# Kernel tuning notes

Hardware: AMD Instinct MI355X
Metric: run time of the kernel (lower is better)

The kernel has to match this reference:

```python
import jax, jax.numpy as jnp
import numpy as np

L, H, DH, D, F, BLK, VOCAB = 2, 16, 128, 2048, 8192, 64, 32000
B, S, R = 16, 77, 16
LORA_SCALE = 32.0 / 16.0  # alpha / r

# standard bitsandbytes NF4 codebook
NF4 = jnp.array([-1.0, -0.6961928009986877, -0.5250730514526367,
                 -0.39491748809814453, -0.28444138169288635, -0.18477343022823334,
                 -0.09105003625154495, 0.0, 0.07958029955625534, 0.16093020141124725,
                 0.24611230194568634, 0.33791524171829224, 0.44070982933044434,
                 0.5626170039176941, 0.723855197429657, 1.0], dtype=jnp.float32)


def setup_inputs() -> dict:
    key = jax.random.key(0)
    ks = jax.random.split(key, 24)
    n = lambda k, sh, s=0.02: jax.random.normal(k, sh, jnp.float32) * s
    u = lambda k, sh: jax.random.uniform(k, sh, dtype=jnp.float32) * 0.02
    ri = lambda k, sh, hi: jax.random.randint(k, sh, 0, hi, jnp.int32)
    return {
        "input_ids": ri(ks[0], (B, S), VOCAB),
        "attention_mask": jnp.ones((B, S), jnp.int32),
        "embed": n(ks[1], (VOCAB, D)),
        "ln_attn": jnp.ones((L, D), jnp.float32),
        "ln_mlp": jnp.ones((L, D), jnp.float32),
        "ln_final": jnp.ones((D,), jnp.float32),
        "qkv_codes": ri(ks[2], (L, 3, D, D), 16),
        "qkv_absmax": u(ks[3], (L, 3, D, D // BLK)),
        "qkv_A": n(ks[4], (L, 3, R, D)),
        "qkv_B": n(ks[5], (L, 3, D, R), 0.01),
        "o_codes": ri(ks[6], (L, D, D), 16),
        "o_absmax": u(ks[7], (L, D, D // BLK)),
        "o_A": n(ks[8], (L, R, D)),
        "o_B": n(ks[9], (L, D, R), 0.01),
        "gu_codes": ri(ks[10], (L, 2, F, D), 16),
        "gu_absmax": u(ks[11], (L, 2, F, D // BLK)),
        "gu_A": n(ks[12], (L, 2, R, D)),
        "gu_B": n(ks[13], (L, 2, F, R), 0.01),
        "down_codes": ri(ks[14], (L, D, F), 16),
        "down_absmax": u(ks[15], (L, D, F // BLK)),
        "down_A": n(ks[16], (L, R, F)),
        "down_B": n(ks[17], (L, D, R), 0.01),
    }


def _rmsnorm(x, w, eps=1e-6):
    return x * jax.lax.rsqrt(jnp.mean(x * x, axis=-1, keepdims=True) + eps) * w


def _dequant(codes, absmax):
    # codes: (out, cin) ints in [0,16); absmax: (out, cin//BLK) blockwise scales
    out, cin = codes.shape
    w = NF4[codes].reshape(out, cin // BLK, BLK) * absmax[..., None]
    return w.reshape(out, cin)


def _qlora(x, codes, absmax, A, Bm):
    # NF4 dequant base matmul + rank-R LoRA delta (eval mode, no dropout)
    W = _dequant(codes, absmax)
    return x @ W.T + LORA_SCALE * ((x @ A.T) @ Bm.T)


def _rope_cache(seq):
    inv = 1.0 / (10000.0 ** (jnp.arange(0, DH, 2, dtype=jnp.float32) / DH))
    f = jnp.arange(seq, dtype=jnp.float32)[:, None] * inv  # (S, DH/2)
    emb = jnp.concatenate([f, f], axis=-1)                 # (S, DH)
    return jnp.cos(emb), jnp.sin(emb)


def _rope(x, cos, sin):
    # x: (B, H, S, DH), llama-style rotate_half
    x1, x2 = jnp.split(x, 2, axis=-1)
    return x * cos + jnp.concatenate([-x2, x1], axis=-1) * sin


def _forward(input_ids, attention_mask, embed, ln_attn, ln_mlp, ln_final,
             qkv_codes, qkv_absmax, qkv_A, qkv_B,
             o_codes, o_absmax, o_A, o_B,
             gu_codes, gu_absmax, gu_A, gu_B,
             down_codes, down_absmax, down_A, down_B):
    b, s = input_ids.shape
    h = embed[input_ids]                                    # (B, S, D)
    cos, sin = _rope_cache(s)
    pad = attention_mask.astype(bool)[:, None, None, :]     # (B,1,1,S)
    mask = pad & jnp.tril(jnp.ones((s, s), bool))
    inv_sqrt_dh = np.float32(1.0 / np.sqrt(DH))
    for l in range(L):
        x = _rmsnorm(h, ln_attn[l])
        q, k, v = [_qlora(x, qkv_codes[l, i], qkv_absmax[l, i], qkv_A[l, i], qkv_B[l, i])
                   .reshape(b, s, H, DH).transpose(0, 2, 1, 3) for i in range(3)]
        q, k = _rope(q, cos, sin), _rope(k, cos, sin)
        scores = jnp.einsum('bhqd,bhkd->bhqk', q, k) * inv_sqrt_dh
        attn = jax.nn.softmax(jnp.where(mask, scores, -1e9), axis=-1)
        o = jnp.einsum('bhqk,bhkd->bhqd', attn, v).transpose(0, 2, 1, 3).reshape(b, s, D)
        h = h + _qlora(o, o_codes[l], o_absmax[l], o_A[l], o_B[l])
        x = _rmsnorm(h, ln_mlp[l])
        g = _qlora(x, gu_codes[l, 0], gu_absmax[l, 0], gu_A[l, 0], gu_B[l, 0])
        up = _qlora(x, gu_codes[l, 1], gu_absmax[l, 1], gu_A[l, 1], gu_B[l, 1])
        h = h + _qlora(jax.nn.silu(g) * up,
                       down_codes[l], down_absmax[l], down_A[l], down_B[l])
    h = _rmsnorm(h, ln_final)
    lengths = attention_mask.sum(axis=1) - 1                # last non-pad token index
    return h[jnp.arange(b), lengths]                        # (B, D)


def reference(input_ids, attention_mask, embed, ln_attn, ln_mlp, ln_final,
              qkv_codes, qkv_absmax, qkv_A, qkv_B,
              o_codes, o_absmax, o_A, o_B,
              gu_codes, gu_absmax, gu_A, gu_B,
              down_codes, down_absmax, down_A, down_B):
    return _forward(input_ids, attention_mask, embed, ln_attn, ln_mlp, ln_final,
                    qkv_codes, qkv_absmax, qkv_A, qkv_B,
                    o_codes, o_absmax, o_A, o_B,
                    gu_codes, gu_absmax, gu_A, gu_B,
                    down_codes, down_absmax, down_A, down_B)
```

## Files before the change

kernel.cpp:

```cpp
#include <hip/hip_runtime.h>
#include <cstdint>
#include <cstddef>

#define M_TOK   1232
#define M_PAD   1280
#define D_MODEL 2048
#define F_FFN   8192
#define SEQ     77
#define BATCH   16
#define NHEAD   16
#define LRANK   16
#define NLAYER  2
#define ATILE   16
#define MWB     512

typedef short bf16x8 __attribute__((ext_vector_type(8)));
typedef float f32x4  __attribute__((ext_vector_type(4)));

__device__ __constant__ float NF4C[16] = {
  -1.0f, -0.6961928009986877f, -0.5250730514526367f, -0.39491748809814453f,
  -0.28444138169288635f, -0.18477343022823334f, -0.09105003625154495f, 0.0f,
  0.07958029955625534f, 0.16093020141124725f, 0.24611230194568634f,
  0.33791524171829224f, 0.44070982933044434f, 0.5626170039176941f,
  0.723855197429657f, 1.0f };

__device__ inline unsigned short f2b(float f) {
  unsigned u = __builtin_bit_cast(unsigned, f);
  u += 0x7FFFu + ((u >> 16) & 1u);
  return (unsigned short)(u >> 16);
}
__device__ inline float b2f(unsigned short s) {
  return __builtin_bit_cast(float, ((unsigned)s) << 16);
}

__global__ __launch_bounds__(256) void mat_w(
    const int* __restrict__ C, const float* __restrict__ AM,
    unsigned short* __restrict__ W, int K, long total8, int ilv)
{
  __shared__ float tb[16];
  if (threadIdx.x < 16) tb[threadIdx.x] = NF4C[threadIdx.x];
  __syncthreads();
  const int KB = K >> 6;
  for (long i = (long)blockIdx.x * 256 + threadIdx.x; i < total8;
       i += (long)gridDim.x * 256) {
    long e = i << 3;
    int rd = (int)(e / K), k = (int)(e - (long)rd * K);
    int srcn = ilv ? ((rd & 1) * F_FFN + (rd >> 1)) : rd;
    float am = AM[(size_t)srcn * KB + (k >> 6)];
    const int4* cp = (const int4*)(C + (size_t)srcn * K + k);
    int4 a = cp[0], b = cp[1];
    uint4 o;
    o.x = (unsigned)f2b(tb[a.x] * am) | ((unsigned)f2b(tb[a.y] * am) << 16);
    o.y = (unsigned)f2b(tb[a.z] * am) | ((unsigned)f2b(tb[a.w] * am) << 16);
    o.z = (unsigned)f2b(tb[b.x] * am) | ((unsigned)f2b(tb[b.y] * am) << 16);
    o.w = (unsigned)f2b(tb[b.z] * am) | ((unsigned)f2b(tb[b.w] * am) << 16);
    *(uint4*)(W + e) = o;
  }
}

__global__ __launch_bounds__(256, 2) void gemm_bf(
    const unsigned short* __restrict__ X, const unsigned short* __restrict__ W,
    float* __restrict__ O, int mb, int N, int K, int acc_mode, int splitk,
    const float* __restrict__ T, const float* __restrict__ Bm, int sh, int nr,
    int gum, unsigned short* __restrict__ GB,
    const int* __restrict__ C2, const float* __restrict__ AM2,
    unsigned short* __restrict__ W2, int K2, long total8_2, int ilv2, int Ggemm)
{
  __shared__ __align__(16) unsigned short xs[128 * 64];
  __shared__ __align__(16) unsigned short ws[128 * 64];

  int tid = threadIdx.x;

  if ((int)blockIdx.x >= Ggemm) {
    if (total8_2 > 0) {
      float* tb = (float*)xs;
      if (tid < 16) tb[tid] = NF4C[tid];
      __syncthreads();
      int nblk2 = gridDim.x - Ggemm;
      const int KB2 = K2 >> 6;
      for (long i = (long)((int)blockIdx.x - Ggemm) * 256 + tid; i < total8_2;
           i += (long)nblk2 * 256) {
        long e = i << 3;
        int rd = (int)(e / K2), k = (int)(e - (long)rd * K2);
        int srcn = ilv2 ? ((rd & 1) * F_FFN + (rd >> 1)) : rd;
        float am = AM2[(size_t)srcn * KB2 + (k >> 6)];
        const int4* cp = (const int4*)(C2 + (size_t)srcn * K2 + k);
        int4 a = cp[0], b = cp[1];
        uint4 o;
        o.x = (unsigned)f2b(tb[a.x] * am) | ((unsigned)f2b(tb[a.y] * am) << 16);
        o.y = (unsigned)f2b(tb[a.z] * am) | ((unsigned)f2b(tb[a.w] * am) << 16);
        o.z = (unsigned)f2b(tb[b.x] * am) | ((unsigned)f2b(tb[b.y] * am) << 16);
        o.w = (unsigned)f2b(tb[b.z] * am) | ((unsigned)f2b(tb[b.w] * am) << 16);
        *(uint4*)(W2 + e) = o;
      }
    }
    return;
  }

  int nwg = Ggemm;
  int q8 = nwg >> 3, r8 = nwg & 7;
  int xcd = blockIdx.x & 7, pos = blockIdx.x >> 3;
  int wgid = (xcd < r8) ? (xcd * (q8 + 1) + pos)
                        : (r8 * (q8 + 1) + (xcd - r8) * q8 + pos);
  int nb = N >> 7;
  int per = mb * nb;
  int slice = wgid / per; int rem = wgid - slice * per;
  int nblk = rem / mb, mblk = rem - nblk * mb;
  int row0 = mblk << 7, col0 = nblk << 7;
  int KBtot = K >> 6, kcnt = KBtot / splitk, kbeg = slice * kcnt;

  int wave = tid >> 6, lane = tid & 63;
  int fr = lane & 15, fg = lane >> 4, s7 = fr & 7;
  int wm = (wave >> 1) * 64, wn = (wave & 1) * 64;
  int xg = lane >> 3;
  int xcol = (((lane & 7) ^ (xg & 7)) << 3);

  const unsigned short* Xbase = X + (size_t)row0 * K + (size_t)kbeg * 64;
  const unsigned short* Wbase = W + (size_t)col0 * K + (size_t)kbeg * 64;

  f32x4 accm[4][4];
  #pragma unroll
  for (int i = 0; i < 4; ++i)
    #pragma unroll
    for (int j = 0; j < 4; ++j) accm[i][j] = (f32x4){0.f, 0.f, 0.f, 0.f};

  auto stage = [&](int t) {
    const unsigned short* xb = Xbase + (size_t)t * 64;
    const unsigned short* wb = Wbase + (size_t)t * 64;
    #pragma unroll
    for (int p2 = 0; p2 < 4; ++p2) {
      int c = wave * 4 + p2;
      const unsigned short* gp = xb + (size_t)(c * 8 + xg) * K + xcol;
      __builtin_amdgcn_global_load_lds(
          (const __attribute__((address_space(1))) unsigned int*)gp,
          (__attribute__((address_space(3))) unsigned int*)(xs + c * 512),
          16, 0, 0);
    }
    #pragma unroll
    for (int p2 = 0; p2 < 4; ++p2) {
      int c = wave * 4 + p2;
      const unsigned short* gp = wb + (size_t)(c * 8 + xg) * K + xcol;
      __builtin_amdgcn_global_load_lds(
          (const __attribute__((address_space(1))) unsigned int*)gp,
          (__attribute__((address_space(3))) unsigned int*)(ws + c * 512),
          16, 0, 0);
    }
  };
  auto compute = [&]() {
    bf16x8 b0[4], b1[4];
    #pragma unroll
    for (int ni = 0; ni < 4; ++ni) {
      const unsigned short* wr = ws + (wn + ni * 16 + fr) * 64;
      b0[ni] = *(const bf16x8*)(wr + ((fg ^ s7) << 3));
      b1[ni] = *(const bf16x8*)(wr + (((4 | fg) ^ s7) << 3));
    }
    #pragma unroll
    for (int mi = 0; mi < 4; ++mi) {
      const unsigned short* xr = xs + (wm + mi * 16 + fr) * 64;
      bf16x8 a0 = *(const bf16x8*)(xr + ((fg ^ s7) << 3));
      bf16x8 a1 = *(const bf16x8*)(xr + (((4 | fg) ^ s7) << 3));
      #pragma unroll
      for (int ni = 0; ni < 4; ++ni) {
        accm[mi][ni] = __builtin_amdgcn_mfma_f32_16x16x32_bf16(
            a0, b0[ni], accm[mi][ni], 0, 0, 0);
        accm[mi][ni] = __builtin_amdgcn_mfma_f32_16x16x32_bf16(
            a1, b1[ni], accm[mi][ni], 0, 0, 0);
      }
    }
  };

  stage(0);
  for (int t = 0; t < kcnt; ++t) {
    __syncthreads();
    compute();
    if (t + 1 < kcnt) {
      __syncthreads();
      stage(t + 1);
    }
  }

  if (gum) {
    float* Tt = (float*)&xs[0];
    float* Bt = (float*)&ws[0];
    __syncthreads();
    for (int idx = tid; idx < 128 * 32; idx += 256) {
      int rr = idx >> 5, c = idx & 31;
      int gm = row0 + rr;
      Tt[idx] = (gm < M_TOK) ? T[(size_t)gm * 32 + c] : 0.f;
    }
    for (int idx = tid; idx < 128 * 16; idx += 256) {
      int rr = idx >> 4, c = idx & 15;
      int type = rr & 1, nrow = (col0 + rr) >> 1;
      Bt[idx] = Bm[((size_t)type * F_FFN + nrow) * LRANK + c];
    }
    __syncthreads();
    #pragma unroll
    for (int mi = 0; mi < 4; ++mi)
      #pragma unroll
      for (int ni = 0; ni < 4; ++ni) {
        int gm0 = row0 + wm + mi * 16 + fg * 4;
        int gnl = wn + ni * 16 + fr;
        #pragma unroll
        for (int r = 0; r < 4; ++r) {
          int gm = gm0 + r;
          float vv = accm[mi][ni][r];
          const float* tr = Tt + (wm + mi * 16 + fg * 4 + r) * 32 + ((gnl & 1) << 4);
          const float* br = Bt + gnl * 16;
          float s = 0.f;
          #pragma unroll
          for (int c = 0; c < 16; ++c) s += tr[c] * br[c];
          vv += 2.0f * s;
          float prt = __shfl_xor(vv, 1);
          if (gm < M_TOK && !(fr & 1)) {
            float sig = 1.0f / (1.0f + expf(-vv));
            GB[(size_t)gm * F_FFN + ((col0 + gnl) >> 1)] = f2b(vv * sig * prt);
          }
        }
      }
    return;
  }

  int doT = (T != nullptr) && (slice == 0);
  float* Tt = (float*)&xs[0];
  float* Bt = (float*)&ws[0];
  if (doT) {
    __syncthreads();
    int toff = (col0 >> sh) << 4;
    for (int idx = tid; idx < 128 * 16; idx += 256) {
      int rr = idx >> 4, c = idx & 15;
      int gm = row0 + rr;
      Tt[idx] = (gm < M_TOK) ? T[(size_t)gm * nr + toff + c] : 0.f;
      Bt[idx] = Bm[(size_t)(col0 + rr) * LRANK + c];
    }
    __syncthreads();
  }

  #pragma unroll
  for (int mi = 0; mi < 4; ++mi)
    #pragma unroll
    for (int ni = 0; ni < 4; ++ni) {
      int gm0 = row0 + wm + mi * 16 + fg * 4;
      int gnl = wn + ni * 16 + fr;
      int gn = col0 + gnl;
      #pragma unroll
      for (int r = 0; r < 4; ++r) {
        int gm = gm0 + r;
        if (gm < M_TOK) {
          size_t idx = (size_t)gm * N + gn;
          float vv = accm[mi][ni][r];
          if (doT) {
            const float* tr = Tt + (wm + mi * 16 + fg * 4 + r) * 16;
            const float* br = Bt + gnl * 16;
            float s = 0.f;
            #pragma unroll
            for (int c = 0; c < 16; ++c) s += tr[c] * br[c];
            vv += 2.0f * s;
          }
          if (splitk > 1)       atomicAdd(&O[idx], vv);
          else if (acc_mode)    O[idx] += vv;
          else                  O[idx] = vv;
        }
      }
    }
}

__global__ __launch_bounds__(256) void lora1(
    const unsigned short* __restrict__ X, const float* __restrict__ A,
    float* __restrict__ T, int K)
{
  int m0 = blockIdx.x * 4, bi = blockIdx.y, nmat = gridDim.y;
  int g = threadIdx.x >> 4, l16 = threadIdx.x & 15;
  const float* ar = A + (size_t)bi * LRANK * K + (size_t)g * K;
  const unsigned short* x0 = X + (size_t)m0 * K;
  float s0 = 0.f, s1 = 0.f, s2 = 0.f, s3 = 0.f;
  for (int kk = l16 * 4; kk < K; kk += 64) {
    float4 av = *(const float4*)(ar + kk);
    ushort4 v0 = *(const ushort4*)(x0 + kk);
    ushort4 v1 = *(const ushort4*)(x0 + K + kk);
    ushort4 v2 = *(const ushort4*)(x0 + 2 * K + kk);
    ushort4 v3 = *(const ushort4*)(x0 + 3 * K + kk);
    s0 += b2f(v0.x)*av.x + b2f(v0.y)*av.y + b2f(v0.z)*av.z + b2f(v0.w)*av.w;
    s1 += b2f(v1.x)*av.x + b2f(v1.y)*av.y + b2f(v1.z)*av.z + b2f(v1.w)*av.w;
    s2 += b2f(v2.x)*av.x + b2f(v2.y)*av.y + b2f(v2.z)*av.z + b2f(v2.w)*av.w;
    s3 += b2f(v3.x)*av.x + b2f(v3.y)*av.y + b2f(v3.z)*av.z + b2f(v3.w)*av.w;
  }
  #pragma unroll
  for (int off = 8; off; off >>= 1) {
    s0 += __shfl_down(s0, off, 16);
    s1 += __shfl_down(s1, off, 16);
    s2 += __shfl_down(s2, off, 16);
    s3 += __shfl_down(s3, off, 16);
  }
  if (l16 == 0) {
    size_t base = ((size_t)m0 * nmat + bi) * LRANK + g;
    size_t rs = (size_t)nmat * LRANK;
    T[base] = s0; T[base + rs] = s1; T[base + 2*rs] = s2; T[base + 3*rs] = s3;
  }
}

__global__ __launch_bounds__(256) void lora2(
    float* __restrict__ O, const float* __restrict__ T,
    const float* __restrict__ Bm, int N, int sh, int nr)
{
  int m0 = blockIdx.y * 8;
  int n = blockIdx.x * 256 + threadIdx.x;
  __shared__ float ts[8 * 48];
  for (int i = threadIdx.x; i < 8 * nr; i += 256)
    ts[(i / nr) * 48 + (i % nr)] = T[(size_t)(m0 + i / nr) * nr + (i % nr)];
  __syncthreads();
  const float4* br = (const float4*)(Bm + (size_t)n * LRANK);
  float4 b0 = br[0], b1 = br[1], b2 = br[2], b3 = br[3];
  int toff = ((n >> sh) << 4);
  #pragma unroll
  for (int mi = 0; mi < 8; ++mi) {
    const float* tsb = ts + mi * 48 + toff;
    float s = b0.x*tsb[0] + b0.y*tsb[1] + b0.z*tsb[2] + b0.w*tsb[3]
            + b1.x*tsb[4] + b1.y*tsb[5] + b1.z*tsb[6] + b1.w*tsb[7]
            + b2.x*tsb[8] + b2.y*tsb[9] + b2.z*tsb[10] + b2.w*tsb[11]
            + b3.x*tsb[12] + b3.y*tsb[13] + b3.z*tsb[14] + b3.w*tsb[15];
    O[(size_t)(m0 + mi) * N + n] += 2.0f * s;
  }
}

__global__ __launch_bounds__(256) void rmsnorm_k(
    const float* __restrict__ H, const float* __restrict__ W,
    unsigned short* __restrict__ X, int D)
{
  int m = blockIdx.x;
  const float* hr = H + (size_t)m * D;
  float s = 0.f;
  for (int i = threadIdx.x; i < D; i += 256) { float v = hr[i]; s += v * v; }
  __shared__ float red[4];
  #pragma unroll
  for (int off = 32; off; off >>= 1) s += __shfl_down(s, off, 64);
  if ((threadIdx.x & 63) == 0) red[threadIdx.x >> 6] = s;
  __syncthreads();
  float tot = red[0] + red[1] + red[2] + red[3];
  float inv = rsqrtf(tot / (float)D + 1e-6f);
  for (int i = threadIdx.x; i < D; i += 256)
    X[(size_t)m * D + i] = f2b(hr[i] * inv * W[i]);
}

__global__ void rope_table(float* __restrict__ cosT, float* __restrict__ sinT)
{
  int idx = blockIdx.x * 64 + threadIdx.x;
  if (idx >= SEQ * 64) return;
  int s = idx >> 6, j = idx & 63;
  float inv = powf(10000.0f, -(float)(2 * j) / 128.0f);
  float f = (float)s * inv;
  cosT[idx] = cosf(f);
  sinT[idx] = sinf(f);
}

__global__ __launch_bounds__(256) void attn_k(
    const float* __restrict__ QKV, const int* __restrict__ amask,
    const float* __restrict__ cosT, const float* __restrict__ sinT,
    unsigned short* __restrict__ O)
{
  int bh = blockIdx.x, it = blockIdx.y;
  int b = bh >> 4, h = bh & (NHEAD - 1);
  const int STR = 3 * D_MODEL;
  __shared__ float ks[SEQ * 132];
  __shared__ float qs[ATILE * 132];
  __shared__ float sc[ATILE * 80];
  __shared__ int am[SEQ];
  const float scale = 0.08838834764831845f;

  const float* Kb = QKV + (size_t)(b * SEQ) * STR + D_MODEL + h * 128;
  for (int idx = threadIdx.x; idx < SEQ * 16; idx += 256) {
    int j = idx >> 4, dq = (idx & 15) << 2;
    float4 a = *(const float4*)(Kb + (size_t)j * STR + dq);
    float4 bb = *(const float4*)(Kb + (size_t)j * STR + dq + 64);
    float4 c4 = *(const float4*)(cosT + j * 64 + dq);
    float4 s4 = *(const float4*)(sinT + j * 64 + dq);
    float* kr = ks + j * 132 + dq;
    kr[0] = a.x*c4.x - bb.x*s4.x; kr[1] = a.y*c4.y - bb.y*s4.y;
    kr[2] = a.z*c4.z - bb.z*s4.z; kr[3] = a.w*c4.w - bb.w*s4.w;
    kr[64] = bb.x*c4.x + a.x*s4.x; kr[65] = bb.y*c4.y + a.y*s4.y;
    kr[66] = bb.z*c4.z + a.z*s4.z; kr[67] = bb.w*c4.w + a.w*s4.w;
  }
  const float* Qb = QKV + (size_t)(b * SEQ) * STR + h * 128;
  for (int idx = threadIdx.x; idx < ATILE * 16; idx += 256) {
    int il = idx >> 4, dq = (idx & 15) << 2;
    int i = it * ATILE + il;
    if (i < SEQ) {
      float4 a = *(const float4*)(Qb + (size_t)i * STR + dq);
      float4 bb = *(const float4*)(Qb + (size_t)i * STR + dq + 64);
      float4 c4 = *(const float4*)(cosT + i * 64 + dq);
      float4 s4 = *(const float4*)(sinT + i * 64 + dq);
      float* qr = qs + il * 132 + dq;
      qr[0] = a.x*c4.x - bb.x*s4.x; qr[1] = a.y*c4.y - bb.y*s4.y;
      qr[2] = a.z*c4.z - bb.z*s4.z; qr[3] = a.w*c4.w - bb.w*s4.w;
      qr[64] = bb.x*c4.x + a.x*s4.x; qr[65] = bb.y*c4.y + a.y*s4.y;
      qr[66] = bb.z*c4.z + a.z*s4.z; qr[67] = bb.w*c4.w + a.w*s4.w;
    }
  }
  for (int j = threadIdx.x; j < SEQ; j += 256) am[j] = amask[b * SEQ + j];
  __syncthreads();

  int wave = threadIdx.x >> 6, lane = threadIdx.x & 63;
  #pragma unroll
  for (int r = 0; r < 4; ++r) {
    int il = wave * 4 + r;
    int i = it * ATILE + il;
    if (i < SEQ) {
      const float4* qr = (const float4*)(qs + il * 132);
      int j1 = lane, j2 = lane + 64;
      float v1 = -1e9f, v2 = -1e9f;
      if (j1 <= i && am[j1]) {
        const float4* kr = (const float4*)(ks + j1 * 132);
        float s = 0.f;
        #pragma unroll 8
        for (int d = 0; d < 32; ++d) {
          float4 a = qr[d], c = kr[d];
          s += a.x*c.x + a.y*c.y + a.z*c.z + a.w*c.w;
        }
        v1 = s * scale;
      }
      if (j2 < SEQ && j2 <= i && am[j2]) {
        const float4* kr = (const float4*)(ks + j2 * 132);
        float s = 0.f;
        #pragma unroll 8
        for (int d = 0; d < 32; ++d) {
          float4 a = qr[d], c = kr[d];
          s += a.x*c.x + a.y*c.y + a.z*c.z + a.w*c.w;
        }
        v2 = s * scale;
      }
      float mx = fmaxf(v1, v2);
      #pragma unroll
      for (int off = 32; off; off >>= 1) mx = fmaxf(mx, __shfl_xor(mx, off));
      float e1 = __expf(v1 - mx);
      float e2 = (j2 < SEQ) ? __expf(v2 - mx) : 0.f;
      float sum = e1 + e2;
      #pragma unroll
      for (int off = 32; off; off >>= 1) sum += __shfl_xor(sum, off);
      float inv = 1.0f / sum;
      sc[il * 80 + j1] = e1 * inv;
      if (j2 < SEQ) sc[il * 80 + j2] = e2 * inv;
    }
  }
  __syncthreads();

  const float* Vbase = QKV + (size_t)(b * SEQ) * STR + 2 * D_MODEL + h * 128;
  for (int idx = threadIdx.x; idx < ATILE * 32; idx += 256) {
    int il = idx >> 5, d4 = (idx & 31) << 2;
    int i = it * ATILE + il;
    if (i >= SEQ) continue;
    float4 acc = {0.f, 0.f, 0.f, 0.f};
    const float* sr = sc + il * 80;
    for (int j = 0; j < SEQ; ++j) {
      float pp = sr[j];
      float4 v = *(const float4*)(Vbase + (size_t)j * STR + d4);
      acc.x += pp * v.x; acc.y += pp * v.y; acc.z += pp * v.z; acc.w += pp * v.w;
    }
    unsigned short* op = O + (size_t)(b * SEQ + i) * D_MODEL + h * 128 + d4;
    op[0] = f2b(acc.x); op[1] = f2b(acc.y); op[2] = f2b(acc.z); op[3] = f2b(acc.w);
  }
}

__global__ void embed_gather(const float* __restrict__ E, const int* __restrict__ ids,
                             float* __restrict__ H)
{
  size_t idx = (size_t)blockIdx.x * 256 + threadIdx.x;
  int m = (int)(idx / D_MODEL);
  int n = (int)(idx % D_MODEL);
  H[idx] = E[(size_t)ids[m] * D_MODEL + n];
}

__global__ __launch_bounds__(256) void final_k(
    const float* __restrict__ H, const int* __restrict__ amask,
    const float* __restrict__ W, float* __restrict__ out)
{
  int b = blockIdx.x;
  __shared__ int len;
  if (threadIdx.x == 0) {
    int s = 0;
    for (int j = 0; j < SEQ; ++j) s += amask[b * SEQ + j];
    len = s - 1;
  }
  __syncthreads();
  const float* hr = H + ((size_t)(b * SEQ + len) * D_MODEL);
  float s = 0.f;
  for (int i = threadIdx.x; i < D_MODEL; i += 256) { float v = hr[i]; s += v * v; }
  __shared__ float red[4];
  #pragma unroll
  for (int off = 32; off; off >>= 1) s += __shfl_down(s, off, 64);
  if ((threadIdx.x & 63) == 0) red[threadIdx.x >> 6] = s;
  __syncthreads();
  float tot = red[0] + red[1] + red[2] + red[3];
  float inv = rsqrtf(tot / (float)D_MODEL + 1e-6f);
  for (int i = threadIdx.x; i < D_MODEL; i += 256)
    out[(size_t)b * D_MODEL + i] = hr[i] * inv * W[i];
}

extern "C" void kernel_launch(void* const* d_in, const int* in_sizes, int n_in,
                              void* d_out, int out_size, void* d_ws, size_t ws_size,
                              hipStream_t stream) {
  const int*   ids     = (const int*)d_in[0];
  const int*   amask   = (const int*)d_in[1];
  const float* embed   = (const float*)d_in[2];
  const float* ln_attn = (const float*)d_in[3];
  const float* ln_mlp  = (const float*)d_in[4];
  const float* ln_fin  = (const float*)d_in[5];
  const int*   qkvC    = (const int*)d_in[6];
  const float* qkvS    = (const float*)d_in[7];
  const float* qkvA    = (const float*)d_in[8];
  const float* qkvB    = (const float*)d_in[9];
  const int*   oC      = (const int*)d_in[10];
  const float* oS      = (const float*)d_in[11];
  const float* oA      = (const float*)d_in[12];
  const float* oB      = (const float*)d_in[13];
  const int*   guC     = (const int*)d_in[14];
  const float* guS     = (const float*)d_in[15];
  const float* guA     = (const float*)d_in[16];
  const float* guB     = (const float*)d_in[17];
  const int*   dnC     = (const int*)d_in[18];
  const float* dnS     = (const float*)d_in[19];
  const float* dnA     = (const float*)d_in[20];
  const float* dnB     = (const float*)d_in[21];
  float* out = (float*)d_out;

  const int M = M_TOK, Mp = M_PAD, D = D_MODEL, F = F_FFN, R = LRANK;
  float* p = (float*)d_ws;
  float* h    = p; p += (size_t)Mp * D;
  float* qkv  = p; p += (size_t)Mp * 3 * D;
  float* t    = p; p += (size_t)Mp * 48;
  float* cosT = p; p += SEQ * 64;
  float* sinT = p; p += SEQ * 64;
  unsigned short* xbf = (unsigned short*)p; p += (size_t)Mp * D / 2;
  unsigned short* gbf = (unsigned short*)p; p += (size_t)Mp * F / 2;
  unsigned short* wQ = (unsigned short*)p; p += (size_t)3 * D * D / 2;
  unsigned short* wO = (unsigned short*)p; p += (size_t)D * D / 2;
  unsigned short* wG = (unsigned short*)p; p += (size_t)2 * F * D / 2;
  unsigned short* wD = (unsigned short*)p; p += (size_t)D * F / 2;

  rope_table<<<(SEQ*64 + 63)/64, 64, 0, stream>>>(cosT, sinT);
  embed_gather<<<(M * D)/256, 256, 0, stream>>>(embed, ids, h);
  mat_w<<<2048, 256, 0, stream>>>(qkvC, qkvS, wQ, D, (long)3*D*D/8, 0);

  const int mb = Mp / 128;
  const int Gqkv = mb * (3*D/128) * 2;
  const int Go   = mb * (D/128) * 4;
  const int Ggu  = mb * (2*F/128);
  const int Gdn  = mb * (D/128) * 8;

  for (int l = 0; l < NLAYER; ++l) {
    rmsnorm_k<<<M, 256, 0, stream>>>(h, ln_attn + (size_t)l * D, xbf, D);
    lora1<<<dim3(M/4, 3), 256, 0, stream>>>(xbf, qkvA + (size_t)l*3*R*D, t, D);
    hipMemsetAsync(qkv, 0, (size_t)Mp * 3 * D * sizeof(float), stream);
    gemm_bf<<<Gqkv + MWB, 256, 0, stream>>>(
        xbf, wQ, qkv, mb, 3*D, D, 0, 2,
        t, qkvB + (size_t)l*3*D*R, 11, 48, 0, nullptr,
        oC + (size_t)l*D*D, oS + (size_t)l*D*(D/64), wO, D, (long)D*D/8, 0, Gqkv);
    attn_k<<<dim3(BATCH*NHEAD, (SEQ + ATILE - 1)/ATILE), 256, 0, stream>>>(
        qkv, amask, cosT, sinT, xbf);
    gemm_bf<<<Go + MWB, 256, 0, stream>>>(
        xbf, wO, h, mb, D, D, 1, 4, nullptr, nullptr, 0, 0, 0, nullptr,
        guC + (size_t)l*2*F*D, guS + (size_t)l*2*F*(D/64), wG, D, (long)2*F*D/8, 1, Go);
    lora1<<<dim3(M/4, 1), 256, 0, stream>>>(xbf, oA + (size_t)l*R*D, t, D);
    lora2<<<dim3(D/256, M/8), 256, 0, stream>>>(h, t, oB + (size_t)l*D*R, D, 11, 16);

    rmsnorm_k<<<M, 256, 0, stream>>>(h, ln_mlp + (size_t)l * D, xbf, D);
    lora1<<<dim3(M/4, 2), 256, 0, stream>>>(xbf, guA + (size_t)l*2*R*D, t, D);
    gemm_bf<<<Ggu + MWB, 256, 0, stream>>>(
        xbf, wG, nullptr, mb, 2*F, D, 0, 1,
        t, guB + (size_t)l*2*F*R, 0, 32, 1, gbf,
        dnC + (size_t)l*D*F, dnS + (size_t)l*D*(F/64), wD, F, (long)D*F/8, 0, Ggu);
    if (l + 1 < NLAYER) {
      gemm_bf<<<Gdn + MWB, 256, 0, stream>>>(
          gbf, wD, h, mb, D, F, 1, 8, nullptr, nullptr, 0, 0, 0, nullptr,
          qkvC + (size_t)(l+1)*3*D*D, qkvS + (size_t)(l+1)*3*D*(D/64),
          wQ, D, (long)3*D*D/8, 0, Gdn);
    } else {
      gemm_bf<<<Gdn, 256, 0, stream>>>(
          gbf, wD, h, mb, D, F, 1, 8, nullptr, nullptr, 0, 0, 0, nullptr,
          nullptr, nullptr, nullptr, D, 0, 0, Gdn);
    }
    lora1<<<dim3(M/4, 1), 256, 0, stream>>>(gbf, dnA + (size_t)l*R*F, t, F);
    lora2<<<dim3(D/256, M/8), 256, 0, stream>>>(h, t, dnB + (size_t)l*D*R, D, 11, 16);
  }
  final_k<<<BATCH, 256, 0, stream>>>(h, amask, ln_fin, out);
}
```

Measured before the change: 1.323 ms.

## Fuse LoRA up-projection into o/down GEMM epilogues and cut split-K

Deletes the separate lora2 kernel and folds the LoRA B-projection for the o and down projections into the gemm_bf epilogue. To make that possible, lora1 for those projections now runs before the GEMM. The split-K factor drops from 2 to 1 for QKV, which lets the qkv memset go away, and from 8 to 4 for down. This saves kernel launches and extra read-modify-write passes over h, but with fewer K-splits there are fewer blocks in flight, and the epilogue with split-K accumulation must add the LoRA term exactly once.

```diff
diff --git a/kernel.cpp b/kernel.cpp
--- a/kernel.cpp
+++ b/kernel.cpp
@@ -295,30 +295,6 @@
     size_t base = ((size_t)m0 * nmat + bi) * LRANK + g;
     size_t rs = (size_t)nmat * LRANK;
     T[base] = s0; T[base + rs] = s1; T[base + 2*rs] = s2; T[base + 3*rs] = s3;
-  }
-}
-
-__global__ __launch_bounds__(256) void lora2(
-    float* __restrict__ O, const float* __restrict__ T,
-    const float* __restrict__ Bm, int N, int sh, int nr)
-{
-  int m0 = blockIdx.y * 8;
-  int n = blockIdx.x * 256 + threadIdx.x;
-  __shared__ float ts[8 * 48];
-  for (int i = threadIdx.x; i < 8 * nr; i += 256)
-    ts[(i / nr) * 48 + (i % nr)] = T[(size_t)(m0 + i / nr) * nr + (i % nr)];
-  __syncthreads();
-  const float4* br = (const float4*)(Bm + (size_t)n * LRANK);
-  float4 b0 = br[0], b1 = br[1], b2 = br[2], b3 = br[3];
-  int toff = ((n >> sh) << 4);
-  #pragma unroll
-  for (int mi = 0; mi < 8; ++mi) {
-    const float* tsb = ts + mi * 48 + toff;
-    float s = b0.x*tsb[0] + b0.y*tsb[1] + b0.z*tsb[2] + b0.w*tsb[3]
-            + b1.x*tsb[4] + b1.y*tsb[5] + b1.z*tsb[6] + b1.w*tsb[7]
-            + b2.x*tsb[8] + b2.y*tsb[9] + b2.z*tsb[10] + b2.w*tsb[11]
-            + b3.x*tsb[12] + b3.y*tsb[13] + b3.z*tsb[14] + b3.w*tsb[15];
-    O[(size_t)(m0 + mi) * N + n] += 2.0f * s;
   }
 }
 
@@ -540,26 +516,25 @@
   mat_w<<<2048, 256, 0, stream>>>(qkvC, qkvS, wQ, D, (long)3*D*D/8, 0);
 
   const int mb = Mp / 128;
-  const int Gqkv = mb * (3*D/128) * 2;
+  const int Gqkv = mb * (3*D/128);
   const int Go   = mb * (D/128) * 4;
   const int Ggu  = mb * (2*F/128);
-  const int Gdn  = mb * (D/128) * 8;
+  const int Gdn  = mb * (D/128) * 4;
 
   for (int l = 0; l < NLAYER; ++l) {
     rmsnorm_k<<<M, 256, 0, stream>>>(h, ln_attn + (size_t)l * D, xbf, D);
     lora1<<<dim3(M/4, 3), 256, 0, stream>>>(xbf, qkvA + (size_t)l*3*R*D, t, D);
-    hipMemsetAsync(qkv, 0, (size_t)Mp * 3 * D * sizeof(float), stream);
     gemm_bf<<<Gqkv + MWB, 256, 0, stream>>>(
-        xbf, wQ, qkv, mb, 3*D, D, 0, 2,
+        xbf, wQ, qkv, mb, 3*D, D, 0, 1,
         t, qkvB + (size_t)l*3*D*R, 11, 48, 0, nullptr,
         oC + (size_t)l*D*D, oS + (size_t)l*D*(D/64), wO, D, (long)D*D/8, 0, Gqkv);
     attn_k<<<dim3(BATCH*NHEAD, (SEQ + ATILE - 1)/ATILE), 256, 0, stream>>>(
         qkv, amask, cosT, sinT, xbf);
+    lora1<<<dim3(M/4, 1), 256, 0, stream>>>(xbf, oA + (size_t)l*R*D, t, D);
     gemm_bf<<<Go + MWB, 256, 0, stream>>>(
-        xbf, wO, h, mb, D, D, 1, 4, nullptr, nullptr, 0, 0, 0, nullptr,
+        xbf, wO, h, mb, D, D, 1, 4,
+        t, oB + (size_t)l*D*R, 11, 16, 0, nullptr,
         guC + (size_t)l*2*F*D, guS + (size_t)l*2*F*(D/64), wG, D, (long)2*F*D/8, 1, Go);
-    lora1<<<dim3(M/4, 1), 256, 0, stream>>>(xbf, oA + (size_t)l*R*D, t, D);
-    lora2<<<dim3(D/256, M/8), 256, 0, stream>>>(h, t, oB + (size_t)l*D*R, D, 11, 16);
 
     rmsnorm_k<<<M, 256, 0, stream>>>(h, ln_mlp + (size_t)l * D, xbf, D);
     lora1<<<dim3(M/4, 2), 256, 0, stream>>>(xbf, guA + (size_t)l*2*R*D, t, D);
@@ -567,18 +542,19 @@
         xbf, wG, nullptr, mb, 2*F, D, 0, 1,
         t, guB + (size_t)l*2*F*R, 0, 32, 1, gbf,
         dnC + (size_t)l*D*F, dnS + (size_t)l*D*(F/64), wD, F, (long)D*F/8, 0, Ggu);
+    lora1<<<dim3(M/4, 1), 256, 0, stream>>>(gbf, dnA + (size_t)l*R*F, t, F);
     if (l + 1 < NLAYER) {
       gemm_bf<<<Gdn + MWB, 256, 0, stream>>>(
-          gbf, wD, h, mb, D, F, 1, 8, nullptr, nullptr, 0, 0, 0, nullptr,
+          gbf, wD, h, mb, D, F, 1, 4,
+          t, dnB + (size_t)l*D*R, 11, 16, 0, nullptr,
           qkvC + (size_t)(l+1)*3*D*D, qkvS + (size_t)(l+1)*3*D*(D/64),
           wQ, D, (long)3*D*D/8, 0, Gdn);
     } else {
       gemm_bf<<<Gdn, 256, 0, stream>>>(
-          gbf, wD, h, mb, D, F, 1, 8, nullptr, nullptr, 0, 0, 0, nullptr,
+          gbf, wD, h, mb, D, F, 1, 4,
+          t, dnB + (size_t)l*D*R, 11, 16, 0, nullptr,
           nullptr, nullptr, nullptr, D, 0, 0, Gdn);
     }
-    lora1<<<dim3(M/4, 1), 256, 0, stream>>>(gbf, dnA + (size_t)l*R*F, t, F);
-    lora2<<<dim3(D/256, M/8), 256, 0, stream>>>(h, t, dnB + (size_t)l*D*R, D, 11, 16);
   }
   final_k<<<BATCH, 256, 0, stream>>>(h, amask, ln_fin, out);
 }
```

After: 1.158 ms. 12.5% less time.
